# Kernel tuning notes

Hardware: AMD Instinct MI355X
Metric: run time of the kernel (lower is better)

The kernel has to match this reference:

```python
import jax, jax.numpy as jnp
import numpy as np
import math

N, E, NF, BF, H, NH, DEPTH = 2048, 65536, 128, 16, 512, 8, 5
HD = H // NH

def _lin(key, fan_in, fan_out):
    k1, k2 = jax.random.split(key)
    W = jax.random.normal(k1, (fan_in, fan_out), jnp.float32) * math.sqrt(2.0 / fan_out)
    b = jnp.zeros((fan_out,), jnp.float32)
    return W, b

def setup_inputs() -> dict:
    key = jax.random.key(0)
    ks = jax.random.split(key, 12)
    x = jax.random.normal(ks[0], (N, NF), jnp.float32)
    edge_index = jax.random.randint(ks[1], (2, E), 0, N, jnp.int64)
    edge_attr = jax.random.normal(ks[2], (E, BF), jnp.float32)
    Wn, bn = _lin(ks[3], NF, H)
    We, be = _lin(ks[4], BF, NH)
    Wq, bq = _lin(ks[5], H, H)
    Wk, bk = _lin(ks[6], H, H)
    Wv, bv = _lin(ks[7], H, H)
    Wo, bo = _lin(ks[8], H, H)
    W1, b1 = _lin(ks[9], H, 4 * H)
    W2, b2 = _lin(ks[10], 4 * H, H)
    g1 = jnp.ones((H,), jnp.float32); be1 = jnp.zeros((H,), jnp.float32)
    g2 = jnp.ones((H,), jnp.float32); be2 = jnp.zeros((H,), jnp.float32)
    return dict(x=x, edge_index=edge_index, edge_attr=edge_attr,
                Wn=Wn, bn=bn, We=We, be=be, Wq=Wq, bq=bq, Wk=Wk, bk=bk,
                Wv=Wv, bv=bv, Wo=Wo, bo=bo, W1=W1, b1=b1, W2=W2, b2=b2,
                g1=g1, be1=be1, g2=g2, be2=be2)

def _ln(x, g, b, eps=1e-5):
    m = jnp.mean(x, axis=-1, keepdims=True)
    v = jnp.var(x, axis=-1, keepdims=True)
    return (x - m) * jax.lax.rsqrt(v + eps) * g + b

def reference(x, edge_index, edge_attr, Wn, bn, We, be, Wq, bq, Wk, bk,
              Wv, bv, Wo, bo, W1, b1, W2, b2, g1, be1, g2, be2):
    h = x @ Wn + bn                                   # [N, H]
    e_bias = edge_attr @ We + be                      # [E, NH]
    src, dst = edge_index[0], edge_index[1]
    bias = jnp.zeros((NH, N, N), jnp.float32).at[:, src, dst].set(e_bias.T)
    scale = 1.0 / math.sqrt(HD)
    for _ in range(DEPTH):
        Q = (h @ Wq + bq).reshape(N, NH, HD).transpose(1, 0, 2)   # [h, n, d]
        K = (h @ Wk + bk).reshape(N, NH, HD).transpose(1, 0, 2)
        V = (h @ Wv + bv).reshape(N, NH, HD).transpose(1, 0, 2)
        scores = jnp.einsum('hnd,hmd->hnm', Q, K) * scale + bias  # [h, n, m]
        attn = jax.nn.softmax(scores, axis=-1)
        out = jnp.einsum('hnm,hmd->hnd', attn, V)                 # [h, n, d]
        out = out.transpose(1, 0, 2).reshape(N, H) @ Wo + bo
        h = _ln(h + out, g1, be1)
        h_ff = jnp.maximum(h @ W1 + b1, 0.0) @ W2 + b2
        h = _ln(h + h_ff, g2, be2)
    return h
```

## Files before the change

kernel.cpp:

```cpp
#include <hip/hip_runtime.h>
#include <hip/hip_bf16.h>

#define NN 2048
#define EE 65536
#define NF_ 128
#define HH 512
#define NHH 8
#define HD 64
#define DEPTH 5
#define KSPLIT 3
#define NTILE_TOT (NN / 64)
#define LOG2E 1.4426950408889634f
#define QSCALE 0.18033688011112042f

typedef __attribute__((ext_vector_type(8))) short bf16x8;
typedef __attribute__((ext_vector_type(4))) float f32x4;

__device__ __forceinline__ ushort f2bf(float x) {
    uint u = __builtin_bit_cast(uint, x);
    u += 0x7fffu + ((u >> 16) & 1u);
    return (ushort)(u >> 16);
}

#define GLD16(gp, lp)                                                          \
    __builtin_amdgcn_global_load_lds(                                          \
        (const __attribute__((address_space(1))) unsigned int*)(gp),           \
        (__attribute__((address_space(3))) unsigned int*)(lp), 16, 0, 0)

template<int BM, int BN, int OUT, int RELU>
__global__ __launch_bounds__(256) void gemm_mfma(const ushort* __restrict__ A,
                                                 const ushort* __restrict__ Bt,
                                                 const float* __restrict__ bias,
                                                 float* __restrict__ C,
                                                 ushort* __restrict__ Cb,
                                                 ushort* __restrict__ qb,
                                                 ushort* __restrict__ kb,
                                                 ushort* __restrict__ vtb,
                                                 int M, int N, int K) {
    constexpr int WM = BM / 2, WN = BN / 2;
    constexpr int MR = BM / 32, NR = BN / 32;
    __shared__ __align__(16) ushort As[2][BM * 64];
    __shared__ __align__(16) ushort Bs[2][BN * 64];
    const int t = threadIdx.x;
    const int w = t >> 6, l = t & 63;
    const int wr = w >> 1, wc = w & 1;
    const int m0 = blockIdx.y * BM, n0 = blockIdx.x * BN;

    f32x4 acc[MR][NR];
#pragma unroll
    for (int m = 0; m < MR; ++m)
#pragma unroll
        for (int n = 0; n < NR; ++n) acc[m][n] = (f32x4){0.f, 0.f, 0.f, 0.f};

    const int srow = t >> 3, sch = t & 7;
    auto stage = [&](int buf, int kt) {
#pragma unroll
        for (int r = 0; r < MR; ++r) {
            int rr = r * 32 + srow;
            int c = sch ^ (rr & 7);
            GLD16(A + (size_t)(m0 + rr) * K + kt * 64 + c * 8,
                  &As[buf][rr * 64 + sch * 8]);
        }
#pragma unroll
        for (int r = 0; r < NR; ++r) {
            int rr = r * 32 + srow;
            int c = sch ^ (rr & 7);
            GLD16(Bt + (size_t)(n0 + rr) * K + kt * 64 + c * 8,
                  &Bs[buf][rr * 64 + sch * 8]);
        }
    };

    stage(0, 0);
    const int NT = K / 64;
    for (int kt = 0; kt < NT; ++kt) {
        __syncthreads();
        if (kt + 1 < NT) stage((kt + 1) & 1, kt + 1);
        const int buf = kt & 1;
#pragma unroll
        for (int kk = 0; kk < 2; ++kk) {
            bf16x8 af[MR], bfr[NR];
#pragma unroll
            for (int m = 0; m < MR; ++m) {
                int R = wr * WM + m * 16 + (l & 15);
                int c = kk * 4 + (l >> 4);
                af[m] = *(const bf16x8*)&As[buf][R * 64 + (c ^ (R & 7)) * 8];
            }
#pragma unroll
            for (int n = 0; n < NR; ++n) {
                int R = wc * WN + n * 16 + (l & 15);
                int c = kk * 4 + (l >> 4);
                bfr[n] = *(const bf16x8*)&Bs[buf][R * 64 + (c ^ (R & 7)) * 8];
            }
#pragma unroll
            for (int m = 0; m < MR; ++m)
#pragma unroll
                for (int n = 0; n < NR; ++n)
                    acc[m][n] = __builtin_amdgcn_mfma_f32_16x16x32_bf16(af[m], bfr[n], acc[m][n], 0, 0, 0);
        }
    }

#pragma unroll
    for (int m = 0; m < MR; ++m) {
        int row = m0 + wr * WM + m * 16 + (l >> 4) * 4;
#pragma unroll
        for (int n = 0; n < NR; ++n) {
            int col = n0 + wc * WN + n * 16 + (l & 15);
            float bv = bias[col];
#pragma unroll
            for (int j = 0; j < 4; ++j) {
                float vv = acc[m][n][j] + bv;
                if (RELU) vv = fmaxf(vv, 0.f);
                int r = row + j;
                if (OUT == 0) {
                    C[(size_t)r * N + col] = vv;
                } else if (OUT == 1) {
                    C[(size_t)r * N + col] = vv;
                    Cb[(size_t)r * N + col] = f2bf(vv);
                } else if (OUT == 2) {
                    Cb[(size_t)r * N + col] = f2bf(vv);
                } else {
                    int type = col >> 9, head = (col >> 6) & 7, dd = col & 63;
                    if (type == 0) qb[((size_t)head * NN + r) * 64 + dd] = f2bf(vv * QSCALE);
                    else if (type == 1) kb[((size_t)head * NN + r) * 64 + dd] = f2bf(vv);
                    else vtb[((size_t)head * 64 + dd) * NN + r] = f2bf(vv);
                }
            }
        }
    }
}

__global__ __launch_bounds__(256) void xcvt(const float* __restrict__ x, ushort* __restrict__ xb, int n) {
    int i = blockIdx.x * 256 + threadIdx.x;
    if (i < n) xb[i] = f2bf(x[i]);
}

__global__ __launch_bounds__(256) void wtrans(const float* __restrict__ W, ushort* __restrict__ WT,
                                              int K, int N, int rowoff) {
    __shared__ float tile[32][33];
    int n0 = blockIdx.x * 32, k0 = blockIdx.y * 32;
    int tc = threadIdx.x & 31, tr = threadIdx.x >> 5;
#pragma unroll
    for (int i = 0; i < 32; i += 8) tile[tr + i][tc] = W[(size_t)(k0 + tr + i) * N + n0 + tc];
    __syncthreads();
#pragma unroll
    for (int i = 0; i < 32; i += 8)
        WT[(size_t)(rowoff + n0 + tr + i) * K + k0 + tc] = f2bf(tile[tc][tr + i]);
}

__global__ __launch_bounds__(256) void bconcat(const float* __restrict__ a, const float* __restrict__ b,
                                               const float* __restrict__ c, float* __restrict__ o) {
    int i = blockIdx.x * 256 + threadIdx.x;
    if (i < 1536) o[i] = i < 512 ? a[i] : (i < 1024 ? b[i - 512] : c[i - 1024]);
}

__global__ __launch_bounds__(256) void ebias_kernel(const float* __restrict__ ea,
                                                    const float* __restrict__ We,
                                                    const float* __restrict__ be,
                                                    float* __restrict__ eb) {
    int e = blockIdx.x * 256 + threadIdx.x;
    float a[16];
#pragma unroll
    for (int i = 0; i < 16; ++i) a[i] = ea[(size_t)e * 16 + i];
#pragma unroll
    for (int j = 0; j < 8; ++j) {
        float s = be[j];
#pragma unroll
        for (int i = 0; i < 16; ++i) s += a[i] * We[i * 8 + j];
        eb[(size_t)e * 8 + j] = s;
    }
}

__global__ __launch_bounds__(256) void amax_kernel(const int* __restrict__ eidx, int* __restrict__ lastE) {
    int e = blockIdx.x * 256 + threadIdx.x;
    int s = eidx[e], d = eidx[EE + e];
    atomicMax(&lastE[s * NN + d], e);
}

__global__ __launch_bounds__(256) void count_kernel(const int* __restrict__ eidx,
                                                    const int* __restrict__ lastE,
                                                    int* __restrict__ cnt) {
    int e = blockIdx.x * 256 + threadIdx.x;
    int s = eidx[e], d = eidx[EE + e];
    if (lastE[s * NN + d] == e) atomicAdd(&cnt[s], 1);
}

__global__ __launch_bounds__(256) void scan2048(const int* __restrict__ cnt,
                                                int* __restrict__ rowptr) {
    __shared__ int sums[256];
    int t = threadIdx.x;
    int loc[8];
    int s = 0;
#pragma unroll
    for (int i = 0; i < 8; ++i) { loc[i] = s; s += cnt[t * 8 + i]; }
    sums[t] = s;
    __syncthreads();
    for (int off = 1; off < 256; off <<= 1) {
        int v = (t >= off) ? sums[t - off] : 0;
        __syncthreads();
        sums[t] += v;
        __syncthreads();
    }
    int base = (t == 0) ? 0 : sums[t - 1];
#pragma unroll
    for (int i = 0; i < 8; ++i) rowptr[t * 8 + i] = base + loc[i];
    if (t == 255) rowptr[NN] = sums[255];
}

__global__ __launch_bounds__(256) void rt_count(const int* __restrict__ eidx,
                                                const int* __restrict__ lastE,
                                                int* __restrict__ cnt2) {
    int e = blockIdx.x * 256 + threadIdx.x;
    int s = eidx[e], d = eidx[EE + e];
    if (lastE[s * NN + d] == e) atomicAdd(&cnt2[s * NTILE_TOT + (d >> 6)], 1);
}

__global__ __launch_bounds__(256) void rt_scan(const int* __restrict__ rowptr,
                                               const int* __restrict__ cnt2,
                                               int* __restrict__ rtptr,
                                               int* __restrict__ rtoff) {
    int row = blockIdx.x * 256 + threadIdx.x;
    if (row >= NN) return;
    int base = rowptr[row];
#pragma unroll
    for (int t = 0; t < NTILE_TOT; ++t) {
        rtptr[row * NTILE_TOT + t] = base;
        rtoff[row * NTILE_TOT + t] = base;
        base += cnt2[row * NTILE_TOT + t];
    }
    if (row == NN - 1) rtptr[NN * NTILE_TOT] = base;
}

__global__ __launch_bounds__(256) void rt_fill(const int* __restrict__ eidx,
                                               const int* __restrict__ lastE,
                                               const float* __restrict__ eb,
                                               int* __restrict__ rtoff,
                                               int* __restrict__ csr_dst,
                                               float* __restrict__ csr_b) {
    int e = blockIdx.x * 256 + threadIdx.x;
    int s = eidx[e], d = eidx[EE + e];
    if (lastE[s * NN + d] == e) {
        int pos = atomicAdd(&rtoff[s * NTILE_TOT + (d >> 6)], 1);
        csr_dst[pos] = d & 63;
#pragma unroll
        for (int j = 0; j < 8; ++j) csr_b[(size_t)pos * 8 + j] = eb[(size_t)e * 8 + j] * LOG2E;
    }
}

template<int BIASLDS>
__global__ __launch_bounds__(256) void attn_mfma(const ushort* __restrict__ qb,
                                                 const ushort* __restrict__ kb,
                                                 const ushort* __restrict__ vtb,
                                                 const int* __restrict__ rtptr,
                                                 const int* __restrict__ csr_dst,
                                                 const float* __restrict__ csr_b,
                                                 float* __restrict__ opart,
                                                 float* __restrict__ Mp,
                                                 float* __restrict__ Sp) {
    const int id = blockIdx.x;
    const int f = (id & 7) * 96 + (id >> 3);
    const int n0 = (f & 31) * 64;
    const int head = (f >> 5) & 7;
    const int ks = f >> 8;
    const int tstart = (ks * 32) / 3, tend = ((ks + 1) * 32) / 3;
    const int t = threadIdx.x;
    const int w = t >> 6, l = t & 63;
    const int lq = l & 15, lg = l >> 4;

    __shared__ __align__(16) ushort Ks2[2][64 * 64];
    __shared__ __align__(16) ushort Vs2[2][64 * 64];
    __shared__ __align__(16) ushort Bb[4][16 * 72];
    __shared__ int Rt[64][12];

    bf16x8 qf0, qf1;
    {
        int r = n0 + w * 16 + lq;
        const ushort* qp = qb + ((size_t)head * NN + r) * HD + lg * 8;
        qf0 = *(const bf16x8*)qp;
        qf1 = *(const bf16x8*)(qp + 32);
    }
    const int ntile = tend - tstart;
    for (int i = t; i < 64 * 12; i += 256) {
        int r = i / 12, c = i % 12;
        if (c <= ntile) Rt[r][c] = rtptr[(n0 + r) * NTILE_TOT + tstart + c];
    }
    float M = -1e30f, S = 0.f;
    f32x4 o[4];
#pragma unroll
    for (int db = 0; db < 4; ++db) o[db] = (f32x4){0.f, 0.f, 0.f, 0.f};

    auto stageK = [&](int buf, int tile) {
        int m0k = tile * 64;
#pragma unroll
        for (int s = 0; s < 2; ++s) {
            int slot = t + s * 256;
            int rr = slot >> 3, blk = slot & 7, sb = blk ^ (rr & 7);
            GLD16(kb + ((size_t)head * NN + m0k + rr) * 64 + sb * 8,
                  &Ks2[buf][rr * 64 + blk * 8]);
        }
    };
    auto stageV = [&](int buf, int tile) {
        int m0k = tile * 64;
#pragma unroll
        for (int s = 0; s < 2; ++s) {
            int slot = t + s * 256;
            int rr = slot >> 3, blk = slot & 7, sb = blk ^ (rr & 7);
            GLD16(vtb + ((size_t)head * 64 + rr) * NN + m0k + sb * 8,
                  &Vs2[buf][rr * 64 + blk * 8]);
        }
    };

    stageK(0, tstart);
    stageV(0, tstart);
    __syncthreads();

    const int sl0 = (((lg << 1) + 0) & 3) * 16 + lq;
    const int sl1 = (((lg << 1) + 1) & 3) * 16 + lq;
    const int hi = lg & 2;

    for (int tt = tstart; tt < tend; ++tt) {
        const int tl = tt - tstart;
        const int cb = tl & 1;
        if (tt + 1 < tend) { stageK(cb ^ 1, tt + 1); stageV(cb ^ 1, tt + 1); }

        const int rq = w * 16 + lq;
        const int p0 = Rt[rq][tl], p1 = Rt[rq][tl + 1];

        if (BIASLDS) {
            for (int i = l; i < 144; i += 64)
                *(uint4*)&Bb[w][i * 8] = (uint4){0, 0, 0, 0};
            if (lg == 0) {
                for (int e = p0; e < p1; ++e)
                    Bb[w][lq * 72 + csr_dst[e]] = f2bf(csr_b[(size_t)e * 8 + head]);
            }
        }

        f32x4 vv[4];
        {
            const ushort* Kb_ = &Ks2[cb][0];
            __builtin_amdgcn_s_setprio(1);
#pragma unroll
            for (int b = 0; b < 4; ++b) {
                int key = b * 16 + lq;
                bf16x8 k0 = *(const bf16x8*)&Kb_[key * 64 + ((lg ^ (key & 7)) * 8)];
                bf16x8 k1 = *(const bf16x8*)&Kb_[key * 64 + (((lg + 4) ^ (key & 7)) * 8)];
                f32x4 s_ = {0.f, 0.f, 0.f, 0.f};
                s_ = __builtin_amdgcn_mfma_f32_16x16x32_bf16(k0, qf0, s_, 0, 0, 0);
                s_ = __builtin_amdgcn_mfma_f32_16x16x32_bf16(k1, qf1, s_, 0, 0, 0);
                vv[b] = s_;
            }
            __builtin_amdgcn_s_setprio(0);
        }

        if (BIASLDS) {
#pragma unroll
            for (int b = 0; b < 4; ++b) {
                uint2 bb = *(const uint2*)&Bb[w][lq * 72 + b * 16 + lg * 4];
                vv[b][0] += __builtin_bit_cast(float, bb.x << 16);
                vv[b][1] += __builtin_bit_cast(float, bb.x & 0xffff0000u);
                vv[b][2] += __builtin_bit_cast(float, bb.y << 16);
                vv[b][3] += __builtin_bit_cast(float, bb.y & 0xffff0000u);
            }
        } else {
            for (int e = p0; e < p1; ++e) {
                int dd = csr_dst[e];
                if (((dd >> 2) & 3) == lg) {
                    float bv = csr_b[(size_t)e * 8 + head];
#pragma unroll
                    for (int b = 0; b < 4; ++b)
#pragma unroll
                        for (int j = 0; j < 4; ++j)
                            vv[b][j] += (b == (dd >> 4) && j == (dd & 3)) ? bv : 0.f;
                }
            }
        }

        float mx = vv[0][0];
#pragma unroll
        for (int b = 0; b < 4; ++b)
#pragma unroll
            for (int j = 0; j < 4; ++j) mx = fmaxf(mx, vv[b][j]);
        mx = fmaxf(mx, __shfl_xor(mx, 16, 64));
        mx = fmaxf(mx, __shfl_xor(mx, 32, 64));
        if (!__all(mx <= M)) {
            float Mn = fmaxf(M, mx);
            float fr = exp2f(M - Mn);
            M = Mn;
            S *= fr;
#pragma unroll
            for (int j = 0; j < 4; ++j) {
                float Fj = __shfl(fr, lg * 4 + j, 64);
                o[0][j] *= Fj; o[1][j] *= Fj; o[2][j] *= Fj; o[3][j] *= Fj;
            }
        }
        float ts = 0.f;
#pragma unroll
        for (int b = 0; b < 4; ++b)
#pragma unroll
            for (int j = 0; j < 4; ++j) { vv[b][j] = exp2f(vv[b][j] - M); ts += vv[b][j]; }
        ts += __shfl_xor(ts, 16, 64);
        ts += __shfl_xor(ts, 32, 64);
        S += ts;

        uint U0, U1, U2, U3, U4, U5, U6, U7;
        asm("v_cvt_pk_bf16_f32 %0, %1, %2" : "=v"(U0) : "v"(vv[0][0]), "v"(vv[0][1]));
        asm("v_cvt_pk_bf16_f32 %0, %1, %2" : "=v"(U1) : "v"(vv[0][2]), "v"(vv[0][3]));
        asm("v_cvt_pk_bf16_f32 %0, %1, %2" : "=v"(U2) : "v"(vv[1][0]), "v"(vv[1][1]));
        asm("v_cvt_pk_bf16_f32 %0, %1, %2" : "=v"(U3) : "v"(vv[1][2]), "v"(vv[1][3]));
        asm("v_cvt_pk_bf16_f32 %0, %1, %2" : "=v"(U4) : "v"(vv[2][0]), "v"(vv[2][1]));
        asm("v_cvt_pk_bf16_f32 %0, %1, %2" : "=v"(U5) : "v"(vv[2][2]), "v"(vv[2][3]));
        asm("v_cvt_pk_bf16_f32 %0, %1, %2" : "=v"(U6) : "v"(vv[3][0]), "v"(vv[3][1]));
        asm("v_cvt_pk_bf16_f32 %0, %1, %2" : "=v"(U7) : "v"(vv[3][2]), "v"(vv[3][3]));

        uint ra, rb;
        ra = (uint)__shfl((int)U0, sl0); rb = (uint)__shfl((int)U2, sl0);
        uint p00 = hi ? rb : ra;
        ra = (uint)__shfl((int)U1, sl0); rb = (uint)__shfl((int)U3, sl0);
        uint p01 = hi ? rb : ra;
        ra = (uint)__shfl((int)U0, sl1); rb = (uint)__shfl((int)U2, sl1);
        uint p02 = hi ? rb : ra;
        ra = (uint)__shfl((int)U1, sl1); rb = (uint)__shfl((int)U3, sl1);
        uint p03 = hi ? rb : ra;
        ra = (uint)__shfl((int)U4, sl0); rb = (uint)__shfl((int)U6, sl0);
        uint p10 = hi ? rb : ra;
        ra = (uint)__shfl((int)U5, sl0); rb = (uint)__shfl((int)U7, sl0);
        uint p11 = hi ? rb : ra;
        ra = (uint)__shfl((int)U4, sl1); rb = (uint)__shfl((int)U6, sl1);
        uint p12 = hi ? rb : ra;
        ra = (uint)__shfl((int)U5, sl1); rb = (uint)__shfl((int)U7, sl1);
        uint p13 = hi ? rb : ra;
        uint4 pu0 = {p00, p01, p02, p03};
        uint4 pu1 = {p10, p11, p12, p13};
        bf16x8 pa0 = __builtin_bit_cast(bf16x8, pu0);
        bf16x8 pa1 = __builtin_bit_cast(bf16x8, pu1);

        {
            const ushort* Vb_ = &Vs2[cb][0];
            __builtin_amdgcn_s_setprio(1);
#pragma unroll
            for (int db = 0; db < 4; ++db) {
                int dim = db * 16 + lq;
                bf16x8 v0 = *(const bf16x8*)&Vb_[dim * 64 + ((lg ^ (dim & 7)) * 8)];
                bf16x8 v1 = *(const bf16x8*)&Vb_[dim * 64 + (((lg + 4) ^ (dim & 7)) * 8)];
                o[db] = __builtin_amdgcn_mfma_f32_16x16x32_bf16(pa0, v0, o[db], 0, 0, 0);
                o[db] = __builtin_amdgcn_mfma_f32_16x16x32_bf16(pa1, v1, o[db], 0, 0, 0);
            }
            __builtin_amdgcn_s_setprio(0);
        }
        __syncthreads();
    }

#pragma unroll
    for (int db = 0; db < 4; ++db)
#pragma unroll
        for (int j = 0; j < 4; ++j) {
            int r = n0 + w * 16 + lg * 4 + j;
            opart[((size_t)ks * NN + r) * HH + head * HD + db * 16 + lq] = o[db][j];
        }
    if (l < 16) {
        int r = n0 + w * 16 + l;
        Mp[((size_t)ks * NHH + head) * NN + r] = M;
        Sp[((size_t)ks * NHH + head) * NN + r] = S;
    }
}

__global__ __launch_bounds__(256) void attn_combine(const float* __restrict__ opart,
                                                    const float* __restrict__ Mp,
                                                    const float* __restrict__ Sp,
                                                    ushort* __restrict__ aob) {
    int i = blockIdx.x * 256 + threadIdx.x;
    int row = i >> 9, col = i & 511;
    int head = col >> 6;
    float m0 = Mp[(size_t)head * NN + row];
    float m1 = Mp[((size_t)NHH + head) * NN + row];
    float m2 = Mp[((size_t)2 * NHH + head) * NN + row];
    float s0 = Sp[(size_t)head * NN + row];
    float s1 = Sp[((size_t)NHH + head) * NN + row];
    float s2 = Sp[((size_t)2 * NHH + head) * NN + row];
    float m = fmaxf(m0, fmaxf(m1, m2));
    float w0 = exp2f(m0 - m), w1 = exp2f(m1 - m), w2 = exp2f(m2 - m);
    float num = opart[(size_t)row * HH + col] * w0
              + opart[((size_t)NN + row) * HH + col] * w1
              + opart[((size_t)2 * NN + row) * HH + col] * w2;
    float den = s0 * w0 + s1 * w1 + s2 * w2;
    aob[i] = f2bf(num / den);
}

template<int BF16OUT>
__global__ __launch_bounds__(256) void ln_kernel(const float* __restrict__ a,
                                                 const float* __restrict__ b,
                                                 const float* __restrict__ g,
                                                 const float* __restrict__ be,
                                                 float* __restrict__ out,
                                                 ushort* __restrict__ outb) {
    int row = blockIdx.x * 4 + (threadIdx.x >> 6);
    int lane = threadIdx.x & 63;
    const float* pa = a + (size_t)row * HH;
    const float* pb = b + (size_t)row * HH;
    float x[8];
    float s = 0.f;
#pragma unroll
    for (int i = 0; i < 8; ++i) { x[i] = pa[lane + i * 64] + pb[lane + i * 64]; s += x[i]; }
#pragma unroll
    for (int off = 32; off > 0; off >>= 1) s += __shfl_xor(s, off, 64);
    float mean = s * (1.f / 512.f);
    float vs = 0.f;
#pragma unroll
    for (int i = 0; i < 8; ++i) { float d = x[i] - mean; vs += d * d; }
#pragma unroll
    for (int off = 32; off > 0; off >>= 1) vs += __shfl_xor(vs, off, 64);
    float rs = rsqrtf(vs * (1.f / 512.f) + 1e-5f);
    float* po = out + (size_t)row * HH;
    ushort* pob = outb + (size_t)row * HH;
#pragma unroll
    for (int i = 0; i < 8; ++i) {
        float v = (x[i] - mean) * rs * g[lane + i * 64] + be[lane + i * 64];
        po[lane + i * 64] = v;
        if (BF16OUT) pob[lane + i * 64] = f2bf(v);
    }
}

extern "C" void kernel_launch(void* const* d_in, const int* in_sizes, int n_in,
                              void* d_out, int out_size, void* d_ws, size_t ws_size,
                              hipStream_t stream) {
    const float* x   = (const float*)d_in[0];
    const int*  eidx = (const int*)d_in[1];
    const float* ea  = (const float*)d_in[2];
    const float* Wn = (const float*)d_in[3];  const float* bn = (const float*)d_in[4];
    const float* We = (const float*)d_in[5];  const float* be = (const float*)d_in[6];
    const float* Wq = (const float*)d_in[7];  const float* bq = (const float*)d_in[8];
    const float* Wk = (const float*)d_in[9];  const float* bk = (const float*)d_in[10];
    const float* Wv = (const float*)d_in[11]; const float* bv = (const float*)d_in[12];
    const float* Wo = (const float*)d_in[13]; const float* bo = (const float*)d_in[14];
    const float* W1 = (const float*)d_in[15]; const float* b1 = (const float*)d_in[16];
    const float* W2 = (const float*)d_in[17]; const float* b2 = (const float*)d_in[18];
    const float* g1 = (const float*)d_in[19]; const float* be1 = (const float*)d_in[20];
    const float* g2 = (const float*)d_in[21]; const float* be2 = (const float*)d_in[22];
    float* out = (float*)d_out;

    char* base = (char*)d_ws;
    size_t off = 0;
    auto carve = [&](size_t bytes) { void* p = base + off; off = (off + bytes + 255) & ~(size_t)255; return p; };
    float*  h    = (float*)carve((size_t)NN * HH * 4);
    ushort* hb   = (ushort*)carve((size_t)NN * HH * 2);
    float*  po   = (float*)carve((size_t)NN * HH * 4);
    ushort* ff1b = (ushort*)carve((size_t)NN * 4 * HH * 2);
    ushort* qb   = (ushort*)carve((size_t)NN * HH * 2);
    ushort* kbf  = (ushort*)carve((size_t)NN * HH * 2);
    ushort* vtb  = (ushort*)carve((size_t)NN * HH * 2);
    ushort* aob  = (ushort*)carve((size_t)NN * HH * 2);
    ushort* xb   = (ushort*)carve((size_t)NN * NF_ * 2);
    ushort* WnT  = (ushort*)carve((size_t)HH * NF_ * 2);
    ushort* WqkvT= (ushort*)carve((size_t)3 * HH * HH * 2);
    ushort* WoT  = (ushort*)carve((size_t)HH * HH * 2);
    ushort* W1T  = (ushort*)carve((size_t)4 * HH * HH * 2);
    ushort* W2T  = (ushort*)carve((size_t)4 * HH * HH * 2);
    float*  bqkv = (float*)carve((size_t)3 * HH * 4);
    float*  eb   = (float*)carve((size_t)EE * NHH * 4);
    float*  csr_b= (float*)carve((size_t)EE * NHH * 4);
    float*  Mp   = (float*)carve((size_t)KSPLIT * NHH * NN * 4);
    float*  Sp   = (float*)carve((size_t)KSPLIT * NHH * NN * 4);
    int* cnt     = (int*)carve((size_t)NN * 4);
    int* rowptr  = (int*)carve((size_t)(NN + 1) * 4);
    int* csr_dst = (int*)carve((size_t)EE * 4);
    int* cnt2    = (int*)carve((size_t)NN * NTILE_TOT * 4);
    int* rtptr   = (int*)carve((size_t)(NN * NTILE_TOT + 1) * 4);
    int* rtoff   = (int*)carve((size_t)NN * NTILE_TOT * 4);
    int* lastE = (int*)po;
    float* opart = (float*)po;

    hipMemsetAsync(lastE, 0xFF, (size_t)NN * NN * 4, stream);
    hipMemsetAsync(cnt, 0, (size_t)NN * 4, stream);
    hipMemsetAsync(cnt2, 0, (size_t)NN * NTILE_TOT * 4, stream);

    xcvt<<<(NN * NF_ + 255) / 256, 256, 0, stream>>>(x, xb, NN * NF_);
    wtrans<<<dim3(HH / 32, NF_ / 32), 256, 0, stream>>>(Wn, WnT, NF_, HH, 0);
    wtrans<<<dim3(HH / 32, HH / 32), 256, 0, stream>>>(Wq, WqkvT, HH, HH, 0);
    wtrans<<<dim3(HH / 32, HH / 32), 256, 0, stream>>>(Wk, WqkvT, HH, HH, 512);
    wtrans<<<dim3(HH / 32, HH / 32), 256, 0, stream>>>(Wv, WqkvT, HH, HH, 1024);
    wtrans<<<dim3(HH / 32, HH / 32), 256, 0, stream>>>(Wo, WoT, HH, HH, 0);
    wtrans<<<dim3(4 * HH / 32, HH / 32), 256, 0, stream>>>(W1, W1T, HH, 4 * HH, 0);
    wtrans<<<dim3(HH / 32, 4 * HH / 32), 256, 0, stream>>>(W2, W2T, 4 * HH, HH, 0);
    bconcat<<<6, 256, 0, stream>>>(bq, bk, bv, bqkv);

    ebias_kernel<<<EE / 256, 256, 0, stream>>>(ea, We, be, eb);
    amax_kernel<<<EE / 256, 256, 0, stream>>>(eidx, lastE);
    count_kernel<<<EE / 256, 256, 0, stream>>>(eidx, lastE, cnt);
    scan2048<<<1, 256, 0, stream>>>(cnt, rowptr);
    rt_count<<<EE / 256, 256, 0, stream>>>(eidx, lastE, cnt2);
    rt_scan<<<NN / 256, 256, 0, stream>>>(rowptr, cnt2, rtptr, rtoff);
    rt_fill<<<EE / 256, 256, 0, stream>>>(eidx, lastE, eb, rtoff, csr_dst, csr_b);

    gemm_mfma<64, 64, 1, 0><<<dim3(HH / 64, NN / 64), 256, 0, stream>>>(
        xb, WnT, bn, h, hb, nullptr, nullptr, nullptr, NN, HH, NF_);

    for (int d = 0; d < DEPTH; ++d) {
        gemm_mfma<64, 64, 3, 0><<<dim3(3 * HH / 64, NN / 64), 256, 0, stream>>>(
            hb, WqkvT, bqkv, nullptr, nullptr, qb, kbf, vtb, NN, 3 * HH, HH);
        if (d & 1)
            attn_mfma<0><<<dim3(32 * NHH * KSPLIT), 256, 0, stream>>>(
                qb, kbf, vtb, rtptr, csr_dst, csr_b, opart, Mp, Sp);
        else
            attn_mfma<1><<<dim3(32 * NHH * KSPLIT), 256, 0, stream>>>(
                qb, kbf, vtb, rtptr, csr_dst, csr_b, opart, Mp, Sp);
        attn_combine<<<NN * HH / 256, 256, 0, stream>>>(opart, Mp, Sp, aob);
        gemm_mfma<32, 64, 0, 0><<<dim3(HH / 64, NN / 32), 256, 0, stream>>>(
            aob, WoT, bo, po, nullptr, nullptr, nullptr, nullptr, NN, HH, HH);
        ln_kernel<1><<<NN / 4, 256, 0, stream>>>(h, po, g1, be1, h, hb);
        gemm_mfma<64, 64, 2, 1><<<dim3(4 * HH / 64, NN / 64), 256, 0, stream>>>(
            hb, W1T, b1, nullptr, ff1b, nullptr, nullptr, nullptr, NN, 4 * HH, HH);
        gemm_mfma<32, 64, 0, 0><<<dim3(HH / 64, NN / 32), 256, 0, stream>>>(
            ff1b, W2T, b2, po, nullptr, nullptr, nullptr, nullptr, NN, HH, 4 * HH);
        float* dst = (d == DEPTH - 1) ? out : h;
        ln_kernel<1><<<NN / 4, 256, 0, stream>>>(h, po, g2, be2, dst, hb);
    }
    (void)in_sizes; (void)n_in; (void)out_size; (void)ws_size;
}
```

Baseline: 596.5 us.

## Load K/V fragments directly from global into registers, dropping LDS staging

The attention kernel no longer stages K and V tiles through double-buffered shared memory. Each wave now loads its own MFMA operand fragments straight from global memory into registers, prefetching the next tile after the current MFMAs. This removes the per-tile __syncthreads and the LDS traffic, and the launch bound asks for 3 blocks per CU. The cost is that all four waves fetch the same K/V data redundantly, relying on the cache. Register pressure also rises from holding 16 prefetched fragments.

```diff
diff --git a/kernel.cpp b/kernel.cpp
--- a/kernel.cpp
+++ b/kernel.cpp
@@ -247,15 +247,15 @@
 }
 
 template<int BIASLDS>
-__global__ __launch_bounds__(256) void attn_mfma(const ushort* __restrict__ qb,
-                                                 const ushort* __restrict__ kb,
-                                                 const ushort* __restrict__ vtb,
-                                                 const int* __restrict__ rtptr,
-                                                 const int* __restrict__ csr_dst,
-                                                 const float* __restrict__ csr_b,
-                                                 float* __restrict__ opart,
-                                                 float* __restrict__ Mp,
-                                                 float* __restrict__ Sp) {
+__global__ __launch_bounds__(256, 3) void attn_mfma(const ushort* __restrict__ qb,
+                                                    const ushort* __restrict__ kb,
+                                                    const ushort* __restrict__ vtb,
+                                                    const int* __restrict__ rtptr,
+                                                    const int* __restrict__ csr_dst,
+                                                    const float* __restrict__ csr_b,
+                                                    float* __restrict__ opart,
+                                                    float* __restrict__ Mp,
+                                                    float* __restrict__ Sp) {
     const int id = blockIdx.x;
     const int f = (id & 7) * 96 + (id >> 3);
     const int n0 = (f & 31) * 64;
@@ -266,8 +266,6 @@
     const int w = t >> 6, l = t & 63;
     const int lq = l & 15, lg = l >> 4;
 
-    __shared__ __align__(16) ushort Ks2[2][64 * 64];
-    __shared__ __align__(16) ushort Vs2[2][64 * 64];
     __shared__ __align__(16) ushort Bb[4][16 * 72];
     __shared__ int Rt[64][12];
 
@@ -283,35 +281,36 @@
         int r = i / 12, c = i % 12;
         if (c <= ntile) Rt[r][c] = rtptr[(n0 + r) * NTILE_TOT + tstart + c];
     }
+    __syncthreads();
+
     float M = -1e30f, S = 0.f;
     f32x4 o[4];
 #pragma unroll
     for (int db = 0; db < 4; ++db) o[db] = (f32x4){0.f, 0.f, 0.f, 0.f};
 
-    auto stageK = [&](int buf, int tile) {
-        int m0k = tile * 64;
-#pragma unroll
-        for (int s = 0; s < 2; ++s) {
-            int slot = t + s * 256;
-            int rr = slot >> 3, blk = slot & 7, sb = blk ^ (rr & 7);
-            GLD16(kb + ((size_t)head * NN + m0k + rr) * 64 + sb * 8,
-                  &Ks2[buf][rr * 64 + blk * 8]);
+    bf16x8 kf0[4], kf1[4], vf0[4], vf1[4];
+    const ushort* kbase0 = kb + ((size_t)head * NN) * 64;
+    const ushort* vbase0 = vtb + (size_t)head * 64 * NN;
+    auto loadK = [&](int tile) {
+        const ushort* p = kbase0 + (size_t)tile * 4096 + lq * 64 + lg * 8;
+#pragma unroll
+        for (int b = 0; b < 4; ++b) {
+            kf0[b] = *(const bf16x8*)(p);
+            kf1[b] = *(const bf16x8*)(p + 32);
+            p += 1024;
         }
     };
-    auto stageV = [&](int buf, int tile) {
-        int m0k = tile * 64;
-#pragma unroll
-        for (int s = 0; s < 2; ++s) {
-            int slot = t + s * 256;
-            int rr = slot >> 3, blk = slot & 7, sb = blk ^ (rr & 7);
-            GLD16(vtb + ((size_t)head * 64 + rr) * NN + m0k + sb * 8,
-                  &Vs2[buf][rr * 64 + blk * 8]);
+    auto loadV = [&](int tile) {
+        const ushort* p = vbase0 + (size_t)lq * NN + tile * 64 + lg * 8;
+#pragma unroll
+        for (int db = 0; db < 4; ++db) {
+            vf0[db] = *(const bf16x8*)(p);
+            vf1[db] = *(const bf16x8*)(p + 32);
+            p += (size_t)16 * NN;
         }
     };
-
-    stageK(0, tstart);
-    stageV(0, tstart);
-    __syncthreads();
+    loadK(tstart);
+    loadV(tstart);
 
     const int sl0 = (((lg << 1) + 0) & 3) * 16 + lq;
     const int sl1 = (((lg << 1) + 1) & 3) * 16 + lq;
@@ -319,9 +318,6 @@
 
     for (int tt = tstart; tt < tend; ++tt) {
         const int tl = tt - tstart;
-        const int cb = tl & 1;
-        if (tt + 1 < tend) { stageK(cb ^ 1, tt + 1); stageV(cb ^ 1, tt + 1); }
-
         const int rq = w * 16 + lq;
         const int p0 = Rt[rq][tl], p1 = Rt[rq][tl + 1];
 
@@ -336,20 +332,17 @@
 
         f32x4 vv[4];
         {
-            const ushort* Kb_ = &Ks2[cb][0];
             __builtin_amdgcn_s_setprio(1);
 #pragma unroll
             for (int b = 0; b < 4; ++b) {
-                int key = b * 16 + lq;
-                bf16x8 k0 = *(const bf16x8*)&Kb_[key * 64 + ((lg ^ (key & 7)) * 8)];
-                bf16x8 k1 = *(const bf16x8*)&Kb_[key * 64 + (((lg + 4) ^ (key & 7)) * 8)];
                 f32x4 s_ = {0.f, 0.f, 0.f, 0.f};
-                s_ = __builtin_amdgcn_mfma_f32_16x16x32_bf16(k0, qf0, s_, 0, 0, 0);
-                s_ = __builtin_amdgcn_mfma_f32_16x16x32_bf16(k1, qf1, s_, 0, 0, 0);
+                s_ = __builtin_amdgcn_mfma_f32_16x16x32_bf16(kf0[b], qf0, s_, 0, 0, 0);
+                s_ = __builtin_amdgcn_mfma_f32_16x16x32_bf16(kf1[b], qf1, s_, 0, 0, 0);
                 vv[b] = s_;
             }
             __builtin_amdgcn_s_setprio(0);
         }
+        if (tt + 1 < tend) loadK(tt + 1);
 
         if (BIASLDS) {
 #pragma unroll
@@ -434,19 +427,15 @@
         bf16x8 pa1 = __builtin_bit_cast(bf16x8, pu1);
 
         {
-            const ushort* Vb_ = &Vs2[cb][0];
             __builtin_amdgcn_s_setprio(1);
 #pragma unroll
             for (int db = 0; db < 4; ++db) {
-                int dim = db * 16 + lq;
-                bf16x8 v0 = *(const bf16x8*)&Vb_[dim * 64 + ((lg ^ (dim & 7)) * 8)];
-                bf16x8 v1 = *(const bf16x8*)&Vb_[dim * 64 + (((lg + 4) ^ (dim & 7)) * 8)];
-                o[db] = __builtin_amdgcn_mfma_f32_16x16x32_bf16(pa0, v0, o[db], 0, 0, 0);
-                o[db] = __builtin_amdgcn_mfma_f32_16x16x32_bf16(pa1, v1, o[db], 0, 0, 0);
+                o[db] = __builtin_amdgcn_mfma_f32_16x16x32_bf16(pa0, vf0[db], o[db], 0, 0, 0);
+                o[db] = __builtin_amdgcn_mfma_f32_16x16x32_bf16(pa1, vf1[db], o[db], 0, 0, 0);
             }
             __builtin_amdgcn_s_setprio(0);
         }
-        __syncthreads();
+        if (tt + 1 < tend) loadV(tt + 1);
     }
 
 #pragma unroll
```

After: 745.8 us. +25.0%, slower.
